# Kernel optimization log

Measured on AMD Instinct MI355X. Metric: run time of the kernel, lower is better.

## Reference

```python
import jax, jax.numpy as jnp
import numpy as np

N = 100000   # nodes
E = 1000000  # edges
IN, H, OUT = 256, 64, 16


def setup_inputs() -> dict:
    key = jax.random.key(0)
    k0, k1, k2, k3 = jax.random.split(key, 4)
    x = jax.random.normal(k0, (N, IN), jnp.float32)
    edge_index = jax.random.randint(k1, (2, E), 0, N)
    # GCNConv parameters (glorot-ish weights, zero bias as in PyG defaults)
    W1 = jax.random.normal(k2, (IN, H), jnp.float32) / np.sqrt(IN).astype(np.float32)
    b1 = jnp.zeros((H,), jnp.float32)
    W2 = jax.random.normal(k3, (H, OUT), jnp.float32) / np.sqrt(H).astype(np.float32)
    b2 = jnp.zeros((OUT,), jnp.float32)
    return {"x": x, "edge_index": edge_index, "W1": W1, "b1": b1, "W2": W2, "b2": b2}


def gcn_conv(x, W, b, src, dst, n):
    # PyG GCNConv: h = x @ W; out[v] = sum_{(u->v)} norm(u,v) * h[u] + b
    h = x @ W                                    # [n, out]
    deg = jnp.zeros((n,), h.dtype).at[dst].add(1.0)
    dinv = jnp.where(deg > 0, jax.lax.rsqrt(deg), 0.0)
    norm = dinv[src] * dinv[dst]                 # [E+n] symmetric normalization
    msg = h[src] * norm[:, None]                 # gather + scale
    agg = jax.ops.segment_sum(msg, dst, num_segments=n)  # scatter-add
    return agg + b


def reference(x, edge_index, W1, b1, W2, b2):
    n = x.shape[0]
    # add self-loops (PyG GCNConv default add_self_loops=True)
    loops = jnp.arange(n, dtype=edge_index.dtype)
    src = jnp.concatenate([edge_index[0], loops])
    dst = jnp.concatenate([edge_index[1], loops])
    h = gcn_conv(x, W1, b1, src, dst, n)
    h = jax.nn.relu(h)  # F.dropout is identity in eval mode (training=False)
    return gcn_conv(h, W2, b2, src, dst, n)
```

## Files before the change

### kernel.cpp

```cpp
#include <hip/hip_runtime.h>

namespace {
constexpr int NN  = 100000;
constexpr int NE  = 1000000;
constexpr int INF = 256;
constexpr int HF  = 64;
constexpr int OF  = 16;
constexpr int SCAN_CHUNK = 1024;
constexpr int NBLK = (NN + SCAN_CHUNK - 1) / SCAN_CHUNK;
constexpr int NSEG = 8;
constexpr int SEGW = (NN + NSEG - 1) / NSEG;
constexpr int CNTW = 100096;
constexpr int ZBLK = (CNTW / 4 + 255) / 256;
constexpr int GB   = (NN + 127) / 128;
constexpr int ECHUNK = 2048;
constexpr int EGRP = (NE + ECHUNK - 1) / ECHUNK;
constexpr int SB   = EGRP * NSEG;
constexpr int SCB  = EGRP;
}

typedef __attribute__((ext_vector_type(8))) short     sh8;
typedef __attribute__((ext_vector_type(4))) float     f32x4;
typedef __attribute__((ext_vector_type(8))) unsigned short us8;

__device__ __forceinline__ unsigned short f2bf(float f) {
    unsigned int u = __builtin_bit_cast(unsigned int, f);
    u += 0x7FFFu + ((u >> 16) & 1u);
    return (unsigned short)(u >> 16);
}
__device__ __forceinline__ float bf2f(unsigned short s) {
    return __builtin_bit_cast(float, (unsigned int)s << 16);
}

__global__ void k_pre(int* __restrict__ cnt, const float* __restrict__ W1,
                      unsigned short* __restrict__ wt_g) {
    int b = blockIdx.x, t = threadIdx.x;
    if (b < ZBLK) {
        int i = (b * 256 + t) * 4;
        if (i < CNTW) *(int4*)(cnt + i) = (int4){0, 0, 0, 0};
    } else {
        int idx = (b - ZBLK) * 256 + t;
        int c = idx >> 8, k = idx & 255;
        wt_g[idx] = f2bf(W1[(size_t)k * HF + c]);
    }
}

__global__ __launch_bounds__(256) void k_hist(const int* __restrict__ dst,
                                              int* __restrict__ cnt,
                                              int* __restrict__ rank) {
    int b   = blockIdx.x;
    int seg = b & (NSEG - 1);
    int grp = b >> 3;
    int e0  = grp * ECHUNK + threadIdx.x;
    int d[8];
    #pragma unroll
    for (int i = 0; i < 8; ++i) {
        int e = e0 + i * 256;
        d[i] = (e < NE) ? dst[e] : -1;
    }
    #pragma unroll
    for (int i = 0; i < 8; ++i) {
        if ((unsigned)d[i] / (unsigned)SEGW == (unsigned)seg)
            rank[e0 + i * 256] = atomicAdd(&cnt[d[i]], 1);
    }
}

__global__ __launch_bounds__(256) void k_reduce(const int* __restrict__ cnt,
                                                int* __restrict__ bsum,
                                                float* __restrict__ dinv) {
    int t = threadIdx.x;
    int i0 = blockIdx.x * SCAN_CHUNK + t * 4;
    int s = 0;
    float dv[4] = {0.f, 0.f, 0.f, 0.f};
    #pragma unroll
    for (int q = 0; q < 4; ++q) {
        if (i0 + q < NN) {
            int c = cnt[i0 + q];
            s += c;
            dv[q] = rsqrtf((float)(c + 1));
        }
    }
    if (i0 + 3 < NN) *(float4*)(dinv + i0) = (float4){dv[0], dv[1], dv[2], dv[3]};
    else { for (int q = 0; q < 4; ++q) if (i0 + q < NN) dinv[i0 + q] = dv[q]; }
    #pragma unroll
    for (int off = 32; off > 0; off >>= 1) s += __shfl_down(s, off);
    __shared__ int wsum[4];
    int lane = t & 63, wid = t >> 6;
    if (lane == 0) wsum[wid] = s;
    __syncthreads();
    if (t == 0) bsum[blockIdx.x] = wsum[0] + wsum[1] + wsum[2] + wsum[3];
}

__global__ __launch_bounds__(256) void k_scan(const int* __restrict__ cnt,
                                              const int* __restrict__ bsum,
                                              int* __restrict__ rowptr) {
    int t = threadIdx.x;
    int b = blockIdx.x;
    int lane = t & 63, wid = t >> 6;

    int p = 0;
    if (lane < b) p += bsum[lane];
    if (64 + lane < b) p += bsum[64 + lane];
    #pragma unroll
    for (int off = 32; off > 0; off >>= 1) p += __shfl_down(p, off);
    int blockBase = __shfl(p, 0);

    int i0 = b * SCAN_CHUNK + t * 4;
    int v0 = 0, v1 = 0, v2 = 0, v3 = 0;
    if (i0 + 0 < NN) v0 = cnt[i0 + 0];
    if (i0 + 1 < NN) v1 = cnt[i0 + 1];
    if (i0 + 2 < NN) v2 = cnt[i0 + 2];
    if (i0 + 3 < NN) v3 = cnt[i0 + 3];
    int tsum = v0 + v1 + v2 + v3;
    int incl = tsum;
    #pragma unroll
    for (int off = 1; off < 64; off <<= 1) {
        int n = __shfl_up(incl, off);
        if (lane >= off) incl += n;
    }
    __shared__ int wsum[4];
    if (lane == 63) wsum[wid] = incl;
    __syncthreads();
    int woff = 0;
    for (int w = 0; w < wid; ++w) woff += wsum[w];
    int excl = woff + (incl - tsum) + blockBase;
    int e0 = excl, e1 = e0 + v0, e2 = e1 + v1, e3 = e2 + v2;
    if (i0 + 0 < NN) rowptr[i0 + 0] = e0;
    if (i0 + 1 < NN) rowptr[i0 + 1] = e1;
    if (i0 + 2 < NN) rowptr[i0 + 2] = e2;
    if (i0 + 3 < NN) rowptr[i0 + 3] = e3;
    if (i0 + 3 == NN - 1) rowptr[NN] = e3 + v3;
}

__global__ __launch_bounds__(256, 8) void k_gs(const float* __restrict__ x,
                                               const unsigned short* __restrict__ wt_g,
                                               unsigned short* __restrict__ h1,
                                               const int* __restrict__ src,
                                               const int* __restrict__ dst,
                                               const int* __restrict__ rank,
                                               const int* __restrict__ rowptr,
                                               int* __restrict__ eidx) {
    int b = blockIdx.x;
    int t = threadIdx.x;

    if (b >= GB) {
        int sb = b - GB;
        int e0 = sb * ECHUNK + t;
        #pragma unroll
        for (int i = 0; i < 8; ++i) {
            int e = e0 + i * 256;
            if (e < NE) {
                int d = dst[e];
                eidx[rowptr[d] + rank[e]] = src[e];
            }
        }
        return;
    }

    int w = t >> 6, l = t & 63;
    int row0 = b * 128;
    int m = l & 15;
    int g = l >> 4;
    int gr0 = row0 + w * 32 + m;      if (gr0 > NN - 1) gr0 = NN - 1;
    int gr1 = row0 + w * 32 + 16 + m; if (gr1 > NN - 1) gr1 = NN - 1;
    const float* p0 = x + (size_t)gr0 * INF + g * 8;
    const float* p1 = x + (size_t)gr1 * INF + g * 8;
    const unsigned short* wb0 = wt_g + (size_t)(0 * 16 + m) * 256 + g * 8;
    const unsigned short* wb1 = wt_g + (size_t)(1 * 16 + m) * 256 + g * 8;
    const unsigned short* wb2 = wt_g + (size_t)(2 * 16 + m) * 256 + g * 8;
    const unsigned short* wb3 = wt_g + (size_t)(3 * 16 + m) * 256 + g * 8;

    f32x4 acc[2][4];
    #pragma unroll
    for (int i = 0; i < 2; ++i)
        #pragma unroll
        for (int j = 0; j < 4; ++j) acc[i][j] = (f32x4){0.f, 0.f, 0.f, 0.f};

    #pragma unroll
    for (int kb = 0; kb < INF; kb += 32) {
        float4 u0 = *(const float4*)(p0 + kb);
        float4 u1 = *(const float4*)(p0 + kb + 4);
        float4 u2 = *(const float4*)(p1 + kb);
        float4 u3 = *(const float4*)(p1 + kb + 4);
        sh8 b0 = *(const sh8*)(wb0 + kb);
        sh8 b1 = *(const sh8*)(wb1 + kb);
        sh8 b2 = *(const sh8*)(wb2 + kb);
        sh8 b3 = *(const sh8*)(wb3 + kb);
        us8 a0u = { f2bf(u0.x), f2bf(u0.y), f2bf(u0.z), f2bf(u0.w),
                    f2bf(u1.x), f2bf(u1.y), f2bf(u1.z), f2bf(u1.w) };
        us8 a1u = { f2bf(u2.x), f2bf(u2.y), f2bf(u2.z), f2bf(u2.w),
                    f2bf(u3.x), f2bf(u3.y), f2bf(u3.z), f2bf(u3.w) };
        sh8 a0 = __builtin_bit_cast(sh8, a0u);
        sh8 a1 = __builtin_bit_cast(sh8, a1u);
        acc[0][0] = __builtin_amdgcn_mfma_f32_16x16x32_bf16(a0, b0, acc[0][0], 0, 0, 0);
        acc[1][0] = __builtin_amdgcn_mfma_f32_16x16x32_bf16(a1, b0, acc[1][0], 0, 0, 0);
        acc[0][1] = __builtin_amdgcn_mfma_f32_16x16x32_bf16(a0, b1, acc[0][1], 0, 0, 0);
        acc[1][1] = __builtin_amdgcn_mfma_f32_16x16x32_bf16(a1, b1, acc[1][1], 0, 0, 0);
        acc[0][2] = __builtin_amdgcn_mfma_f32_16x16x32_bf16(a0, b2, acc[0][2], 0, 0, 0);
        acc[1][2] = __builtin_amdgcn_mfma_f32_16x16x32_bf16(a1, b2, acc[1][2], 0, 0, 0);
        acc[0][3] = __builtin_amdgcn_mfma_f32_16x16x32_bf16(a0, b3, acc[0][3], 0, 0, 0);
        acc[1][3] = __builtin_amdgcn_mfma_f32_16x16x32_bf16(a1, b3, acc[1][3], 0, 0, 0);
    }

    #pragma unroll
    for (int mt = 0; mt < 2; ++mt) {
        #pragma unroll
        for (int r = 0; r < 4; ++r) {
            int gr = row0 + w * 32 + mt * 16 + (l >> 4) * 4 + r;
            if (gr < NN) {
                #pragma unroll
                for (int nt = 0; nt < 4; ++nt)
                    h1[(size_t)gr * HF + nt * 16 + (l & 15)] = f2bf(acc[mt][nt][r]);
            }
        }
    }
}

__global__ __launch_bounds__(256) void k_gather1(const int* __restrict__ rowptr,
                                                 const int* __restrict__ eidx,
                                                 const float* __restrict__ dinv,
                                                 const unsigned short* __restrict__ h1,
                                                 const float* __restrict__ b1,
                                                 const float* __restrict__ W2,
                                                 unsigned short* __restrict__ h2) {
    __shared__ float w2L[HF * OF];
    __shared__ float hrL[32][HF + 4];
    int t = threadIdx.x;
    *(float4*)(w2L + t * 4) = *(const float4*)(W2 + t * 4);

    int nodeL = t >> 3;
    int fg    = t & 7;
    int v     = blockIdx.x * 32 + nodeL;
    int beg = rowptr[v], end = rowptr[v + 1];

    float acc[8] = {};
    int   s_n = 0;  float w_n = 0.f;  us8 h_n = {};
    if (beg < end) {
        s_n = eidx[beg];
        w_n = dinv[s_n];
        h_n = *(const us8*)(h1 + (size_t)s_n * HF + fg * 8);
    }
    for (int i = beg; i < end; ++i) {
        float w_c = w_n;  us8 h_c = h_n;
        if (i + 1 < end) {
            s_n = eidx[i + 1];
            w_n = dinv[s_n];
            h_n = *(const us8*)(h1 + (size_t)s_n * HF + fg * 8);
        }
        #pragma unroll
        for (int q = 0; q < 8; ++q) acc[q] += w_c * bf2f(h_c[q]);
    }

    {
        float dv = dinv[v], sl = dv * dv;
        us8 hv = *(const us8*)(h1 + (size_t)v * HF + fg * 8);
        #pragma unroll
        for (int q = 0; q < 8; ++q) {
            float val = dv * acc[q] + sl * bf2f(hv[q]) + b1[fg * 8 + q];
            hrL[nodeL][fg * 8 + q] = val > 0.f ? val : 0.f;
        }
    }
    __syncthreads();

    #pragma unroll
    for (int T = t; T < 512; T += 256) {
        int n = T >> 4, j = T & 15;
        const float* hr = hrL[n];
        float p = 0.f;
        #pragma unroll
        for (int k = 0; k < HF; ++k) p += hr[k] * w2L[k * OF + j];
        h2[(size_t)(blockIdx.x * 32 + n) * OF + j] = f2bf(p);
    }
}

__global__ __launch_bounds__(256) void k_gather2(const int* __restrict__ rowptr,
                                                 const int* __restrict__ eidx,
                                                 const float* __restrict__ dinv,
                                                 const unsigned short* __restrict__ h2,
                                                 const float* __restrict__ b2,
                                                 float* __restrict__ out) {
    int t     = threadIdx.x;
    int nodeL = t >> 4;
    int j     = t & 15;
    int v     = blockIdx.x * 16 + nodeL;
    int beg = rowptr[v], end = rowptr[v + 1];

    float acc = 0.f;
    int   s_n = 0;  float w_n = 0.f;  unsigned short h_n = 0;
    if (beg < end) {
        s_n = eidx[beg];
        w_n = dinv[s_n];
        h_n = h2[(size_t)s_n * OF + j];
    }
    for (int i = beg; i < end; ++i) {
        float w_c = w_n;  unsigned short h_c = h_n;
        if (i + 1 < end) {
            s_n = eidx[i + 1];
            w_n = dinv[s_n];
            h_n = h2[(size_t)s_n * OF + j];
        }
        acc += w_c * bf2f(h_c);
    }
    float dv = dinv[v];
    out[(size_t)v * OF + j] = dv * acc + dv * dv * bf2f(h2[(size_t)v * OF + j]) + b2[j];
}

extern "C" void kernel_launch(void* const* d_in, const int* in_sizes, int n_in,
                              void* d_out, int out_size, void* d_ws, size_t ws_size,
                              hipStream_t stream) {
    const float* x   = (const float*)d_in[0];
    const int*   ei  = (const int*)d_in[1];
    const int*   src = ei;
    const int*   dst = ei + NE;
    const float* W1  = (const float*)d_in[2];
    const float* b1  = (const float*)d_in[3];
    const float* W2  = (const float*)d_in[4];
    const float* b2  = (const float*)d_in[5];
    float* out = (float*)d_out;

    float* dinv  = (float*)d_ws;
    unsigned short* h1b = (unsigned short*)(dinv + CNTW);
    unsigned short* h2b = (unsigned short*)(h1b + (size_t)NN * HF);
    int*   cnt   = (int*)(h2b + (size_t)NN * OF + (size_t)NN * OF);
    int*   rowptr = cnt + CNTW;
    int*   rank  = rowptr + 100352;
    int*   eidx  = rank + NE;
    int*   bsum  = eidx + NE;
    unsigned short* wt_g = (unsigned short*)(bsum + 128);

    k_pre<<<ZBLK + 64, 256, 0, stream>>>(cnt, W1, wt_g);
    k_hist<<<SB, 256, 0, stream>>>(dst, cnt, rank);
    k_reduce<<<NBLK, 256, 0, stream>>>(cnt, bsum, dinv);
    k_scan<<<NBLK, 256, 0, stream>>>(cnt, bsum, rowptr);

    k_gs<<<GB + SCB, 256, 0, stream>>>(x, wt_g, h1b, src, dst, rank, rowptr, eidx);

    k_gather1<<<NN / 32, 256, 0, stream>>>(rowptr, eidx, dinv, h1b, b1, W2, h2b);

    k_gather2<<<NN / 16, 256, 0, stream>>>(rowptr, eidx, dinv, h2b, b2, out);
}
```

Before: 174.0 us.

## Stage x tiles into LDS via direct global-to-LDS loads with double buffering

The x@W1 projection in k_gs no longer has each lane load its x rows straight into registers. A block now cooperatively streams 128x32 fp32 tiles into a double-buffered shared-memory array using global_load_lds, with an XOR swizzle so the LDS reads avoid bank conflicts. The next K-slice is prefetched while MFMAs run on the current one, with a barrier at the end of each iteration. The aim is fully coalesced x reads and overlap of load latency with compute. The costs are 32KB of LDS per block, extra barriers, a launch-bounds drop from 8 to 4, and LDS allocated even by the edge-scatter blocks that share this kernel.

```diff
diff --git a/kernel.cpp b/kernel.cpp
--- a/kernel.cpp
+++ b/kernel.cpp
@@ -32,6 +32,12 @@
     return __builtin_bit_cast(float, (unsigned int)s << 16);
 }
 
+__device__ __forceinline__ void gload_lds16(const void* g, void* l) {
+    __builtin_amdgcn_global_load_lds(
+        (const __attribute__((address_space(1))) void*)g,
+        (__attribute__((address_space(3))) void*)l, 16, 0, 0);
+}
+
 __global__ void k_pre(int* __restrict__ cnt, const float* __restrict__ W1,
                       unsigned short* __restrict__ wt_g) {
     int b = blockIdx.x, t = threadIdx.x;
@@ -132,7 +138,7 @@
     if (i0 + 3 == NN - 1) rowptr[NN] = e3 + v3;
 }
 
-__global__ __launch_bounds__(256, 8) void k_gs(const float* __restrict__ x,
+__global__ __launch_bounds__(256, 4) void k_gs(const float* __restrict__ x,
                                                const unsigned short* __restrict__ wt_g,
                                                unsigned short* __restrict__ h1,
                                                const int* __restrict__ src,
@@ -140,6 +146,7 @@
                                                const int* __restrict__ rank,
                                                const int* __restrict__ rowptr,
                                                int* __restrict__ eidx) {
+    __shared__ float xs[2][128 * 32];
     int b = blockIdx.x;
     int t = threadIdx.x;
 
@@ -161,10 +168,6 @@
     int row0 = b * 128;
     int m = l & 15;
     int g = l >> 4;
-    int gr0 = row0 + w * 32 + m;      if (gr0 > NN - 1) gr0 = NN - 1;
-    int gr1 = row0 + w * 32 + 16 + m; if (gr1 > NN - 1) gr1 = NN - 1;
-    const float* p0 = x + (size_t)gr0 * INF + g * 8;
-    const float* p1 = x + (size_t)gr1 * INF + g * 8;
     const unsigned short* wb0 = wt_g + (size_t)(0 * 16 + m) * 256 + g * 8;
     const unsigned short* wb1 = wt_g + (size_t)(1 * 16 + m) * 256 + g * 8;
     const unsigned short* wb2 = wt_g + (size_t)(2 * 16 + m) * 256 + g * 8;
@@ -176,20 +179,44 @@
         #pragma unroll
         for (int j = 0; j < 4; ++j) acc[i][j] = (f32x4){0.f, 0.f, 0.f, 0.f};
 
-    #pragma unroll
-    for (int kb = 0; kb < INF; kb += 32) {
-        float4 u0 = *(const float4*)(p0 + kb);
-        float4 u1 = *(const float4*)(p0 + kb + 4);
-        float4 u2 = *(const float4*)(p1 + kb);
-        float4 u3 = *(const float4*)(p1 + kb + 4);
+    auto stage = [&](int s) {
+        int kb = s * 32;
+        #pragma unroll
+        for (int p = 0; p < 4; ++p) {
+            int q  = p * 256 + t;
+            int r  = q >> 3;
+            int gs = q & 7;
+            int gr = row0 + r; if (gr > NN - 1) gr = NN - 1;
+            const float* srcp = x + (size_t)gr * INF + kb + ((gs ^ (r & 7)) << 2);
+            gload_lds16(srcp, &xs[s & 1][q * 4]);
+        }
+    };
+
+    stage(0);
+    __syncthreads();
+
+    int r0 = w * 32 + m;
+    int r1 = r0 + 16;
+    int x0 = ((2 * g) ^ (r0 & 7)) << 2;
+    int x1 = ((2 * g + 1) ^ (r0 & 7)) << 2;
+
+    #pragma unroll
+    for (int s = 0; s < 8; ++s) {
+        if (s + 1 < 8) stage(s + 1);
+        const float* bufp = xs[s & 1];
+        float4 c00 = *(const float4*)(bufp + r0 * 32 + x0);
+        float4 c01 = *(const float4*)(bufp + r0 * 32 + x1);
+        float4 c10 = *(const float4*)(bufp + r1 * 32 + x0);
+        float4 c11 = *(const float4*)(bufp + r1 * 32 + x1);
+        int kb = s * 32;
         sh8 b0 = *(const sh8*)(wb0 + kb);
         sh8 b1 = *(const sh8*)(wb1 + kb);
         sh8 b2 = *(const sh8*)(wb2 + kb);
         sh8 b3 = *(const sh8*)(wb3 + kb);
-        us8 a0u = { f2bf(u0.x), f2bf(u0.y), f2bf(u0.z), f2bf(u0.w),
-                    f2bf(u1.x), f2bf(u1.y), f2bf(u1.z), f2bf(u1.w) };
-        us8 a1u = { f2bf(u2.x), f2bf(u2.y), f2bf(u2.z), f2bf(u2.w),
-                    f2bf(u3.x), f2bf(u3.y), f2bf(u3.z), f2bf(u3.w) };
+        us8 a0u = { f2bf(c00.x), f2bf(c00.y), f2bf(c00.z), f2bf(c00.w),
+                    f2bf(c01.x), f2bf(c01.y), f2bf(c01.z), f2bf(c01.w) };
+        us8 a1u = { f2bf(c10.x), f2bf(c10.y), f2bf(c10.z), f2bf(c10.w),
+                    f2bf(c11.x), f2bf(c11.y), f2bf(c11.z), f2bf(c11.w) };
         sh8 a0 = __builtin_bit_cast(sh8, a0u);
         sh8 a1 = __builtin_bit_cast(sh8, a1u);
         acc[0][0] = __builtin_amdgcn_mfma_f32_16x16x32_bf16(a0, b0, acc[0][0], 0, 0, 0);
@@ -200,6 +227,7 @@
         acc[1][2] = __builtin_amdgcn_mfma_f32_16x16x32_bf16(a1, b2, acc[1][2], 0, 0, 0);
         acc[0][3] = __builtin_amdgcn_mfma_f32_16x16x32_bf16(a0, b3, acc[0][3], 0, 0, 0);
         acc[1][3] = __builtin_amdgcn_mfma_f32_16x16x32_bf16(a1, b3, acc[1][3], 0, 0, 0);
+        __syncthreads();
     }
 
     #pragma unroll
```

New measurement: 167.7 us. 1.04x faster.

## Pre-convert x to bf16 alongside histogram kernel before the MFMA GEMM

Applied to the files above, without the earlier changes.

Adds a conversion pass that casts x from fp32 to bf16 into workspace, fused into the histogram launch so the two can overlap. The GEMM kernel then reads bf16 x directly, halving its input bytes and skipping per-load conversion. The conversion reads the full 100 MB of fp32 x and writes 50 MB, so total traffic rises unless the overlap with the atomic-heavy histogram hides it. A fallback to the old fp32 path is kept for when the workspace is too small.

```diff
diff --git a/kernel.cpp b/kernel.cpp
--- a/kernel.cpp
+++ b/kernel.cpp
@@ -17,6 +17,19 @@
 constexpr int EGRP = (NE + ECHUNK - 1) / ECHUNK;
 constexpr int SB   = EGRP * NSEG;
 constexpr int SCB  = EGRP;
+constexpr int CVB  = (NN * INF) / (256 * 16);
+
+constexpr size_t OFF_dinv = 0;
+constexpr size_t OFF_h1   = OFF_dinv + CNTW;
+constexpr size_t OFF_h2   = OFF_h1 + (size_t)NN * HF / 2;
+constexpr size_t OFF_cnt  = OFF_h2 + (size_t)NN * OF / 2;
+constexpr size_t OFF_rp   = OFF_cnt + CNTW;
+constexpr size_t OFF_rank = OFF_rp + 100352;
+constexpr size_t OFF_eidx = OFF_rank + (size_t)NE;
+constexpr size_t OFF_bsum = OFF_eidx + (size_t)NE;
+constexpr size_t OFF_wtg  = OFF_bsum + 128;
+constexpr size_t OFF_xb   = OFF_wtg + 8192;
+constexpr size_t NEED_XB  = (OFF_xb + (size_t)NN * INF / 2) * 4;
 }
 
 typedef __attribute__((ext_vector_type(8))) short     sh8;
@@ -45,24 +58,53 @@
     }
 }
 
+__device__ __forceinline__ void hist_body(int hb, int t,
+                                          const int* __restrict__ dst,
+                                          int* __restrict__ cnt,
+                                          int* __restrict__ rank) {
+    int seg = hb & (NSEG - 1);
+    int grp = hb >> 3;
+    int e0  = grp * ECHUNK + t;
+    int d[8];
+    #pragma unroll
+    for (int i = 0; i < 8; ++i) {
+        int e = e0 + i * 256;
+        d[i] = (e < NE) ? dst[e] : -1;
+    }
+    #pragma unroll
+    for (int i = 0; i < 8; ++i) {
+        if ((unsigned)d[i] / (unsigned)SEGW == (unsigned)seg)
+            rank[e0 + i * 256] = atomicAdd(&cnt[d[i]], 1);
+    }
+}
+
+__global__ __launch_bounds__(256) void k_hc(const float* __restrict__ x,
+                                            unsigned short* __restrict__ xb,
+                                            const int* __restrict__ dst,
+                                            int* __restrict__ cnt,
+                                            int* __restrict__ rank) {
+    int b = blockIdx.x, t = threadIdx.x;
+    if (b < CVB) {
+        size_t idx = ((size_t)b * 256 + t) * 16;
+        float4 v0 = *(const float4*)(x + idx);
+        float4 v1 = *(const float4*)(x + idx + 4);
+        float4 v2 = *(const float4*)(x + idx + 8);
+        float4 v3 = *(const float4*)(x + idx + 12);
+        us8 lo = { f2bf(v0.x), f2bf(v0.y), f2bf(v0.z), f2bf(v0.w),
+                   f2bf(v1.x), f2bf(v1.y), f2bf(v1.z), f2bf(v1.w) };
+        us8 hi = { f2bf(v2.x), f2bf(v2.y), f2bf(v2.z), f2bf(v2.w),
+                   f2bf(v3.x), f2bf(v3.y), f2bf(v3.z), f2bf(v3.w) };
+        *(us8*)(xb + idx)     = lo;
+        *(us8*)(xb + idx + 8) = hi;
+        return;
+    }
+    hist_body(b - CVB, t, dst, cnt, rank);
+}
+
 __global__ __launch_bounds__(256) void k_hist(const int* __restrict__ dst,
                                               int* __restrict__ cnt,
                                               int* __restrict__ rank) {
-    int b   = blockIdx.x;
-    int seg = b & (NSEG - 1);
-    int grp = b >> 3;
-    int e0  = grp * ECHUNK + threadIdx.x;
-    int d[8];
-    #pragma unroll
-    for (int i = 0; i < 8; ++i) {
-        int e = e0 + i * 256;
-        d[i] = (e < NE) ? dst[e] : -1;
-    }
-    #pragma unroll
-    for (int i = 0; i < 8; ++i) {
-        if ((unsigned)d[i] / (unsigned)SEGW == (unsigned)seg)
-            rank[e0 + i * 256] = atomicAdd(&cnt[d[i]], 1);
-    }
+    hist_body(blockIdx.x, threadIdx.x, dst, cnt, rank);
 }
 
 __global__ __launch_bounds__(256) void k_reduce(const int* __restrict__ cnt,
@@ -132,7 +174,24 @@
     if (i0 + 3 == NN - 1) rowptr[NN] = e3 + v3;
 }
 
-__global__ __launch_bounds__(256, 8) void k_gs(const float* __restrict__ x,
+__device__ __forceinline__ void scatter_body(int sb, int t,
+                                             const int* __restrict__ src,
+                                             const int* __restrict__ dst,
+                                             const int* __restrict__ rank,
+                                             const int* __restrict__ rowptr,
+                                             int* __restrict__ eidx) {
+    int e0 = sb * ECHUNK + t;
+    #pragma unroll
+    for (int i = 0; i < 8; ++i) {
+        int e = e0 + i * 256;
+        if (e < NE) {
+            int d = dst[e];
+            eidx[rowptr[d] + rank[e]] = src[e];
+        }
+    }
+}
+
+__global__ __launch_bounds__(256, 8) void k_gs(const unsigned short* __restrict__ xb,
                                                const unsigned short* __restrict__ wt_g,
                                                unsigned short* __restrict__ h1,
                                                const int* __restrict__ src,
@@ -143,19 +202,70 @@
     int b = blockIdx.x;
     int t = threadIdx.x;
 
-    if (b >= GB) {
-        int sb = b - GB;
-        int e0 = sb * ECHUNK + t;
-        #pragma unroll
-        for (int i = 0; i < 8; ++i) {
-            int e = e0 + i * 256;
-            if (e < NE) {
-                int d = dst[e];
-                eidx[rowptr[d] + rank[e]] = src[e];
+    if (b >= GB) { scatter_body(b - GB, t, src, dst, rank, rowptr, eidx); return; }
+
+    int w = t >> 6, l = t & 63;
+    int row0 = b * 128;
+    int m = l & 15;
+    int g = l >> 4;
+    int gr0 = row0 + w * 32 + m;      if (gr0 > NN - 1) gr0 = NN - 1;
+    int gr1 = row0 + w * 32 + 16 + m; if (gr1 > NN - 1) gr1 = NN - 1;
+    const unsigned short* xp0 = xb + (size_t)gr0 * INF + g * 8;
+    const unsigned short* xp1 = xb + (size_t)gr1 * INF + g * 8;
+    const unsigned short* wb0 = wt_g + (size_t)(0 * 16 + m) * 256 + g * 8;
+    const unsigned short* wb1 = wt_g + (size_t)(1 * 16 + m) * 256 + g * 8;
+    const unsigned short* wb2 = wt_g + (size_t)(2 * 16 + m) * 256 + g * 8;
+    const unsigned short* wb3 = wt_g + (size_t)(3 * 16 + m) * 256 + g * 8;
+
+    f32x4 acc[2][4];
+    #pragma unroll
+    for (int i = 0; i < 2; ++i)
+        #pragma unroll
+        for (int j = 0; j < 4; ++j) acc[i][j] = (f32x4){0.f, 0.f, 0.f, 0.f};
+
+    #pragma unroll
+    for (int kb = 0; kb < INF; kb += 32) {
+        sh8 a0 = *(const sh8*)(xp0 + kb);
+        sh8 a1 = *(const sh8*)(xp1 + kb);
+        sh8 b0 = *(const sh8*)(wb0 + kb);
+        sh8 b1 = *(const sh8*)(wb1 + kb);
+        sh8 b2 = *(const sh8*)(wb2 + kb);
+        sh8 b3 = *(const sh8*)(wb3 + kb);
+        acc[0][0] = __builtin_amdgcn_mfma_f32_16x16x32_bf16(a0, b0, acc[0][0], 0, 0, 0);
+        acc[1][0] = __builtin_amdgcn_mfma_f32_16x16x32_bf16(a1, b0, acc[1][0], 0, 0, 0);
+        acc[0][1] = __builtin_amdgcn_mfma_f32_16x16x32_bf16(a0, b1, acc[0][1], 0, 0, 0);
+        acc[1][1] = __builtin_amdgcn_mfma_f32_16x16x32_bf16(a1, b1, acc[1][1], 0, 0, 0);
+        acc[0][2] = __builtin_amdgcn_mfma_f32_16x16x32_bf16(a0, b2, acc[0][2], 0, 0, 0);
+        acc[1][2] = __builtin_amdgcn_mfma_f32_16x16x32_bf16(a1, b2, acc[1][2], 0, 0, 0);
+        acc[0][3] = __builtin_amdgcn_mfma_f32_16x16x32_bf16(a0, b3, acc[0][3], 0, 0, 0);
+        acc[1][3] = __builtin_amdgcn_mfma_f32_16x16x32_bf16(a1, b3, acc[1][3], 0, 0, 0);
+    }
+
+    #pragma unroll
+    for (int mt = 0; mt < 2; ++mt) {
+        #pragma unroll
+        for (int r = 0; r < 4; ++r) {
+            int gr = row0 + w * 32 + mt * 16 + (l >> 4) * 4 + r;
+            if (gr < NN) {
+                #pragma unroll
+                for (int nt = 0; nt < 4; ++nt)
+                    h1[(size_t)gr * HF + nt * 16 + (l & 15)] = f2bf(acc[mt][nt][r]);
             }
         }
-        return;
-    }
+    }
+}
+
+__global__ __launch_bounds__(256, 8) void k_gs32(const float* __restrict__ x,
+                                                 const unsigned short* __restrict__ wt_g,
+                                                 unsigned short* __restrict__ h1,
+                                                 const int* __restrict__ src,
+                                                 const int* __restrict__ dst,
+                                                 const int* __restrict__ rank,
+                                                 const int* __restrict__ rowptr,
+                                                 int* __restrict__ eidx) {
+    int b = blockIdx.x;
+    int t = threadIdx.x;
+    if (b >= GB) { scatter_body(b - GB, t, src, dst, rank, rowptr, eidx); return; }
 
     int w = t >> 6, l = t & 63;
     int row0 = b * 128;
@@ -318,24 +428,37 @@
     const float* b2  = (const float*)d_in[5];
     float* out = (float*)d_out;
 
-    float* dinv  = (float*)d_ws;
-    unsigned short* h1b = (unsigned short*)(dinv + CNTW);
-    unsigned short* h2b = (unsigned short*)(h1b + (size_t)NN * HF);
-    int*   cnt   = (int*)(h2b + (size_t)NN * OF + (size_t)NN * OF);
-    int*   rowptr = cnt + CNTW;
-    int*   rank  = rowptr + 100352;
-    int*   eidx  = rank + NE;
-    int*   bsum  = eidx + NE;
-    unsigned short* wt_g = (unsigned short*)(bsum + 128);
+    int* ws = (int*)d_ws;
+    float* dinv   = (float*)(ws + OFF_dinv);
+    unsigned short* h1b = (unsigned short*)(ws + OFF_h1);
+    unsigned short* h2b = (unsigned short*)(ws + OFF_h2);
+    int*   cnt    = ws + OFF_cnt;
+    int*   rowptr = ws + OFF_rp;
+    int*   rank   = ws + OFF_rank;
+    int*   eidx   = ws + OFF_eidx;
+    int*   bsum   = ws + OFF_bsum;
+    unsigned short* wt_g = (unsigned short*)(ws + OFF_wtg);
+    unsigned short* xb   = (unsigned short*)(ws + OFF_xb);
+
+    bool use_xb = ws_size >= NEED_XB;
 
     k_pre<<<ZBLK + 64, 256, 0, stream>>>(cnt, W1, wt_g);
-    k_hist<<<SB, 256, 0, stream>>>(dst, cnt, rank);
+
+    if (use_xb) {
+        k_hc<<<CVB + SB, 256, 0, stream>>>(x, xb, dst, cnt, rank);
+    } else {
+        k_hist<<<SB, 256, 0, stream>>>(dst, cnt, rank);
+    }
+
     k_reduce<<<NBLK, 256, 0, stream>>>(cnt, bsum, dinv);
     k_scan<<<NBLK, 256, 0, stream>>>(cnt, bsum, rowptr);
 
-    k_gs<<<GB + SCB, 256, 0, stream>>>(x, wt_g, h1b, src, dst, rank, rowptr, eidx);
+    if (use_xb) {
+        k_gs<<<GB + SCB, 256, 0, stream>>>(xb, wt_g, h1b, src, dst, rank, rowptr, eidx);
+    } else {
+        k_gs32<<<GB + SCB, 256, 0, stream>>>(x, wt_g, h1b, src, dst, rank, rowptr, eidx);
+    }
 
     k_gather1<<<NN / 32, 256, 0, stream>>>(rowptr, eidx, dinv, h1b, b1, W2, h2b);
-
     k_gather2<<<NN / 16, 256, 0, stream>>>(rowptr, eidx, dinv, h2b, b2, out);
 }
```

Result: slower. 182.9 us (+5.1%).

## Split W1 GEMM output columns across waves with smaller row blocks

Applied to the files above, without the earlier changes.

Each block of the fused GEMM/scatter kernel now handles 32 rows instead of 128, and each wave computes one 16-column slice of the 64 outputs instead of all columns for its own 32 rows. This quadruples the GEMM block count and cuts accumulator registers, aiming for higher occupancy and better load balancing. In exchange, all four waves read and convert the same x rows to bf16, which relies on cache hits and repeats the conversion work.

```diff
diff --git a/kernel.cpp b/kernel.cpp
--- a/kernel.cpp
+++ b/kernel.cpp
@@ -12,7 +12,7 @@
 constexpr int SEGW = (NN + NSEG - 1) / NSEG;
 constexpr int CNTW = 100096;
 constexpr int ZBLK = (CNTW / 4 + 255) / 256;
-constexpr int GB   = (NN + 127) / 128;
+constexpr int GB   = (NN + 31) / 32;
 constexpr int ECHUNK = 2048;
 constexpr int EGRP = (NE + ECHUNK - 1) / ECHUNK;
 constexpr int SB   = EGRP * NSEG;
@@ -158,23 +158,17 @@
     }
 
     int w = t >> 6, l = t & 63;
-    int row0 = b * 128;
+    int row0 = b * 32;
     int m = l & 15;
     int g = l >> 4;
-    int gr0 = row0 + w * 32 + m;      if (gr0 > NN - 1) gr0 = NN - 1;
-    int gr1 = row0 + w * 32 + 16 + m; if (gr1 > NN - 1) gr1 = NN - 1;
+    int gr0 = row0 + m;      if (gr0 > NN - 1) gr0 = NN - 1;
+    int gr1 = row0 + 16 + m; if (gr1 > NN - 1) gr1 = NN - 1;
     const float* p0 = x + (size_t)gr0 * INF + g * 8;
     const float* p1 = x + (size_t)gr1 * INF + g * 8;
-    const unsigned short* wb0 = wt_g + (size_t)(0 * 16 + m) * 256 + g * 8;
-    const unsigned short* wb1 = wt_g + (size_t)(1 * 16 + m) * 256 + g * 8;
-    const unsigned short* wb2 = wt_g + (size_t)(2 * 16 + m) * 256 + g * 8;
-    const unsigned short* wb3 = wt_g + (size_t)(3 * 16 + m) * 256 + g * 8;
-
-    f32x4 acc[2][4];
-    #pragma unroll
-    for (int i = 0; i < 2; ++i)
-        #pragma unroll
-        for (int j = 0; j < 4; ++j) acc[i][j] = (f32x4){0.f, 0.f, 0.f, 0.f};
+    const unsigned short* wb = wt_g + (size_t)(w * 16 + m) * 256 + g * 8;
+
+    f32x4 acc0 = (f32x4){0.f, 0.f, 0.f, 0.f};
+    f32x4 acc1 = (f32x4){0.f, 0.f, 0.f, 0.f};
 
     #pragma unroll
     for (int kb = 0; kb < INF; kb += 32) {
@@ -182,37 +176,26 @@
         float4 u1 = *(const float4*)(p0 + kb + 4);
         float4 u2 = *(const float4*)(p1 + kb);
         float4 u3 = *(const float4*)(p1 + kb + 4);
-        sh8 b0 = *(const sh8*)(wb0 + kb);
-        sh8 b1 = *(const sh8*)(wb1 + kb);
-        sh8 b2 = *(const sh8*)(wb2 + kb);
-        sh8 b3 = *(const sh8*)(wb3 + kb);
+        sh8 bb = *(const sh8*)(wb + kb);
         us8 a0u = { f2bf(u0.x), f2bf(u0.y), f2bf(u0.z), f2bf(u0.w),
                     f2bf(u1.x), f2bf(u1.y), f2bf(u1.z), f2bf(u1.w) };
         us8 a1u = { f2bf(u2.x), f2bf(u2.y), f2bf(u2.z), f2bf(u2.w),
                     f2bf(u3.x), f2bf(u3.y), f2bf(u3.z), f2bf(u3.w) };
         sh8 a0 = __builtin_bit_cast(sh8, a0u);
         sh8 a1 = __builtin_bit_cast(sh8, a1u);
-        acc[0][0] = __builtin_amdgcn_mfma_f32_16x16x32_bf16(a0, b0, acc[0][0], 0, 0, 0);
-        acc[1][0] = __builtin_amdgcn_mfma_f32_16x16x32_bf16(a1, b0, acc[1][0], 0, 0, 0);
-        acc[0][1] = __builtin_amdgcn_mfma_f32_16x16x32_bf16(a0, b1, acc[0][1], 0, 0, 0);
-        acc[1][1] = __builtin_amdgcn_mfma_f32_16x16x32_bf16(a1, b1, acc[1][1], 0, 0, 0);
-        acc[0][2] = __builtin_amdgcn_mfma_f32_16x16x32_bf16(a0, b2, acc[0][2], 0, 0, 0);
-        acc[1][2] = __builtin_amdgcn_mfma_f32_16x16x32_bf16(a1, b2, acc[1][2], 0, 0, 0);
-        acc[0][3] = __builtin_amdgcn_mfma_f32_16x16x32_bf16(a0, b3, acc[0][3], 0, 0, 0);
-        acc[1][3] = __builtin_amdgcn_mfma_f32_16x16x32_bf16(a1, b3, acc[1][3], 0, 0, 0);
-    }
-
-    #pragma unroll
-    for (int mt = 0; mt < 2; ++mt) {
-        #pragma unroll
-        for (int r = 0; r < 4; ++r) {
-            int gr = row0 + w * 32 + mt * 16 + (l >> 4) * 4 + r;
-            if (gr < NN) {
-                #pragma unroll
-                for (int nt = 0; nt < 4; ++nt)
-                    h1[(size_t)gr * HF + nt * 16 + (l & 15)] = f2bf(acc[mt][nt][r]);
-            }
-        }
+        acc0 = __builtin_amdgcn_mfma_f32_16x16x32_bf16(a0, bb, acc0, 0, 0, 0);
+        acc1 = __builtin_amdgcn_mfma_f32_16x16x32_bf16(a1, bb, acc1, 0, 0, 0);
+    }
+
+    #pragma unroll
+    for (int r = 0; r < 4; ++r) {
+        int gr = row0 + g * 4 + r;
+        if (gr < NN) h1[(size_t)gr * HF + w * 16 + m] = f2bf(acc0[r]);
+    }
+    #pragma unroll
+    for (int r = 0; r < 4; ++r) {
+        int gr = row0 + 16 + g * 4 + r;
+        if (gr < NN) h1[(size_t)gr * HF + w * 16 + m] = f2bf(acc1[r]);
     }
 }
 
@@ -318,14 +301,14 @@
     const float* b2  = (const float*)d_in[5];
     float* out = (float*)d_out;
 
-    float* dinv  = (float*)d_ws;
+    float* dinv   = (float*)d_ws;
     unsigned short* h1b = (unsigned short*)(dinv + CNTW);
     unsigned short* h2b = (unsigned short*)(h1b + (size_t)NN * HF);
-    int*   cnt   = (int*)(h2b + (size_t)NN * OF + (size_t)NN * OF);
+    int*   cnt    = (int*)(h2b + (size_t)NN * OF + (size_t)NN * OF);
     int*   rowptr = cnt + CNTW;
-    int*   rank  = rowptr + 100352;
-    int*   eidx  = rank + NE;
-    int*   bsum  = eidx + NE;
+    int*   rank   = rowptr + 100352;
+    int*   eidx   = rank + NE;
+    int*   bsum   = eidx + NE;
     unsigned short* wt_g = (unsigned short*)(bsum + 128);
 
     k_pre<<<ZBLK + 64, 256, 0, stream>>>(cnt, W1, wt_g);
```

After: 204.7 us. 17.6% more time.
